# Kernel tuning notes

Measured on AMD Instinct MI355X. Metric: run time of the kernel, lower is better.

The kernel has to match this reference:

```python
import jax, jax.numpy as jnp
import numpy as np

EPS_BN = 1e-5
EPS_NORM = 1e-12


def _l2norm_c(x):
    # F.normalize over channel dim (dim=1) of [n, d, h, w]
    n = jnp.sqrt(jnp.sum(x * x, axis=1, keepdims=True))
    return x / jnp.maximum(n, EPS_NORM)


def setup_inputs() -> dict:
    key = jax.random.key(0)
    ks = jax.random.split(key, 8)
    g, p, d, h, w = 64, 64, 512, 24, 8
    hw = h * w
    return {
        "gal_fea": jax.random.normal(ks[0], (g, d, h, w), dtype=jnp.float32),
        "prob_fea": jax.random.normal(ks[1], (p, d, h, w), dtype=jnp.float32),
        "bn_weight": jax.random.uniform(ks[2], (1,), dtype=jnp.float32) + 0.5,
        "bn_bias": jax.random.uniform(ks[3], (1,), dtype=jnp.float32) - 0.5,
        "bn_mean": jnp.zeros((1,), dtype=jnp.float32),
        "bn_var": jnp.ones((1,), dtype=jnp.float32),
        "fc_weight": jax.random.normal(ks[4], (1, 2 * hw), dtype=jnp.float32) * 0.05,
        "fc_bias": jax.random.normal(ks[5], (1,), dtype=jnp.float32) * 0.05,
        "lbn_weight": jax.random.uniform(ks[6], (1,), dtype=jnp.float32) + 0.5,
        "lbn_bias": jax.random.uniform(ks[7], (1,), dtype=jnp.float32) - 0.5,
        "lbn_mean": jnp.zeros((1,), dtype=jnp.float32),
        "lbn_var": jnp.ones((1,), dtype=jnp.float32),
    }


def reference(gal_fea, prob_fea, bn_weight, bn_bias, bn_mean, bn_var,
              fc_weight, fc_bias, lbn_weight, lbn_bias, lbn_mean, lbn_var):
    g, d, h, w = gal_fea.shape
    p = prob_fea.shape[0]
    hw = h * w

    # L2-normalize over channels, flatten spatial dims
    gal = _l2norm_c(gal_fea).reshape(g, d, hw)              # [g, d, j]
    ker = _l2norm_c(prob_fea).transpose(0, 2, 3, 1).reshape(p, hw, d)  # [p, i, d]

    # cosine-similarity cross-correlation: s[g,p,i,j] = <probe pos i, gallery pos j>
    s = jnp.einsum('pid,gdj->gpij', ker, gal)               # [g, p, hw, hw]

    # dual spatial max-pool: max over probe positions, max over gallery positions
    score = jnp.concatenate([s.max(axis=2), s.max(axis=3)], axis=-1)  # [g, p, 2*hw]

    # eval-mode BatchNorm1d(1): scalar affine broadcast over all elements
    score = (score - bn_mean) / jnp.sqrt(bn_var + EPS_BN) * bn_weight + bn_bias

    # fc: Linear(2*hw, 1)
    score = jnp.einsum('gpk,ok->gpo', score, fc_weight)[..., 0] + fc_bias[0]  # [g, p]

    # eval-mode logit BatchNorm1d(1): scalar affine
    score = (score - lbn_mean) / jnp.sqrt(lbn_var + EPS_BN) * lbn_weight + lbn_bias

    return jax.nn.sigmoid(score / 10.0)
```

## Files before the change

kernel.cpp:

```cpp
#include <hip/hip_runtime.h>

#define HW 192
#define DD 512
#define GG 64
#define PP 64
#define SLAB 98304

typedef __attribute__((ext_vector_type(4))) int intx4;

__device__ __forceinline__ unsigned int pk4(float a, float b, float c, float d) {
  int qa = (int)rintf(a), qb = (int)rintf(b), qc = (int)rintf(c), qd = (int)rintf(d);
  return (unsigned)(qa & 255) | ((unsigned)(qb & 255) << 8) |
         ((unsigned)(qc & 255) << 16) | ((unsigned)(qd & 255) << 24);
}

__global__ __launch_bounds__(512, 2) void norm_kernel(
    const float* __restrict__ gal, const float* __restrict__ prob,
    unsigned char* __restrict__ ws) {
  int b = blockIdx.x;
  int s = b / 12;
  int q = b - s * 12;
  const float* in = (s < GG) ? (gal + (size_t)s * DD * HW)
                             : (prob + (size_t)(s - GG) * DD * HW);
  unsigned char* out = ws + (size_t)s * SLAB;
  int pos0 = q * 16;
  int t = threadIdx.x;

  __shared__ float T[16][524];
  __shared__ float sqa[128][17];
  __shared__ float sq2[16][17];
  __shared__ float scl[16];

  {
    int cq = t >> 2;
    int quad = t & 3;
    float p0 = 0.f, p1 = 0.f, p2 = 0.f, p3 = 0.f;
#pragma unroll
    for (int cb = 0; cb < 4; ++cb) {
      int c = cb * 128 + cq;
      const float4 v = *(const float4*)(in + (size_t)c * HW + pos0 + quad * 4);
      T[quad * 4 + 0][c] = v.x;
      T[quad * 4 + 1][c] = v.y;
      T[quad * 4 + 2][c] = v.z;
      T[quad * 4 + 3][c] = v.w;
      p0 += v.x * v.x; p1 += v.y * v.y; p2 += v.z * v.z; p3 += v.w * v.w;
    }
    sqa[cq][quad * 4 + 0] = p0;
    sqa[cq][quad * 4 + 1] = p1;
    sqa[cq][quad * 4 + 2] = p2;
    sqa[cq][quad * 4 + 3] = p3;
  }
  __syncthreads();
  if (t < 256) {
    int g2 = t >> 4, pos = t & 15;
    float v = 0.f;
#pragma unroll
    for (int r = 0; r < 8; ++r) v += sqa[g2 * 8 + r][pos];
    sq2[g2][pos] = v;
  }
  __syncthreads();
  if (t < 16) {
    float v = 0.f;
#pragma unroll
    for (int r = 0; r < 16; ++r) v += sq2[r][t];
    scl[t] = 1.f / fmaxf(sqrtf(v), 1e-12f);
  }
  __syncthreads();

  {
    int kb2 = t >> 6;
    int lane = t & 63;
    int l4 = lane >> 4;
    int pos = lane & 15;
    float sc = scl[pos] * 127.f;
    int base = kb2 * 64 + l4 * 16;
    const float4 r0 = *(const float4*)&T[pos][base + 0];
    const float4 r1 = *(const float4*)&T[pos][base + 4];
    const float4 r2 = *(const float4*)&T[pos][base + 8];
    const float4 r3 = *(const float4*)&T[pos][base + 12];
    uint4 u;
    u.x = pk4(r0.x * sc, r0.y * sc, r0.z * sc, r0.w * sc);
    u.y = pk4(r1.x * sc, r1.y * sc, r1.z * sc, r1.w * sc);
    u.z = pk4(r2.x * sc, r2.y * sc, r2.z * sc, r2.w * sc);
    u.w = pk4(r3.x * sc, r3.y * sc, r3.z * sc, r3.w * sc);
    *(uint4*)(out + (size_t)kb2 * 12288 + (size_t)q * 1024 + (size_t)lane * 16) = u;
  }
}

#define GLOAD_LDS16(gp, lp)                                              \
  __builtin_amdgcn_global_load_lds(                                      \
      (const __attribute__((address_space(1))) unsigned int*)(gp),       \
      (__attribute__((address_space(3))) unsigned int*)(lp), 16, 0, 0)

__global__ __launch_bounds__(256, 2) void qaconv_gemm(
    const unsigned char* __restrict__ ws, const float* __restrict__ fcw,
    const float* __restrict__ bnw, const float* __restrict__ bnb,
    const float* __restrict__ bnm, const float* __restrict__ bnv,
    const float* __restrict__ fcb, const float* __restrict__ lw,
    const float* __restrict__ lb, const float* __restrict__ lm,
    const float* __restrict__ lv, float* __restrict__ out) {
  int bid0 = blockIdx.x;
  int bid = ((bid0 & 7) << 9) + (bid0 >> 3);
  int sb = bid >> 6, li = bid & 63;
  int g = ((sb >> 3) << 3) + (li >> 3);
  int p = ((sb & 7) << 3) + (li & 7);
  const unsigned char* Bsrc = ws + (size_t)g * SLAB;
  const unsigned char* Asrc = ws + (size_t)(GG + p) * SLAB;

  __shared__ unsigned char sbuf[3][24576];

  int tid = threadIdx.x;
  int lane = tid & 63;
  int wave = tid >> 6;
  int wi = wave >> 1, wj = wave & 1;
  int l15 = lane & 15, l4 = lane >> 4;

  intx4 acc[6][6];
#pragma unroll
  for (int a = 0; a < 6; ++a)
#pragma unroll
    for (int c = 0; c < 6; ++c) acc[a][c] = (intx4){0, 0, 0, 0};

  const unsigned char* stgsrc =
      ((wave < 2) ? Asrc : Bsrc) + (size_t)((wave & 1) * 6) * 1024 +
      (size_t)lane * 16;
  int fbase = wave * 6;

#define STAGE(KB)                                                         \
  do {                                                                    \
    const unsigned char* s_ = stgsrc + (size_t)(KB)*12288;                \
    _Pragma("unroll") for (int i_ = 0; i_ < 6; ++i_) {                    \
      GLOAD_LDS16(s_ + i_ * 1024, &sbuf[(KB) % 3][(fbase + i_) * 1024]);  \
    }                                                                     \
  } while (0)

  intx4 aR[2][6], bR[2][6];

#define DSRD(KB, RB)                                                      \
  do {                                                                    \
    const unsigned char* cb_ = &sbuf[(KB) % 3][lane * 16];                \
    _Pragma("unroll") for (int i_ = 0; i_ < 6; ++i_) {                    \
      aR[RB][i_] = *(const intx4*)(cb_ + (wi * 6 + i_) * 1024);           \
      bR[RB][i_] = *(const intx4*)(cb_ + (12 + wj * 6 + i_) * 1024);      \
    }                                                                     \
  } while (0)

#define MFMAB(RB)                                                         \
  do {                                                                    \
    _Pragma("unroll") for (int jt_ = 0; jt_ < 6; ++jt_) {                 \
      intx4 bb = bR[RB][jt_];                                             \
      _Pragma("unroll") for (int it_ = 0; it_ < 6; ++it_)                 \
          acc[it_][jt_] = __builtin_amdgcn_mfma_i32_16x16x64_i8(          \
              aR[RB][it_], bb, acc[it_][jt_], 0, 0, 0);                   \
    }                                                                     \
  } while (0)

#define PHASE(KB, VMW)                                                    \
  do {                                                                    \
    asm volatile("s_waitcnt vmcnt(" #VMW ") lgkmcnt(0)" ::: "memory");    \
    __builtin_amdgcn_s_barrier();                                         \
    if ((KB) + 3 <= 7) STAGE((KB) + 3);                                   \
    if ((KB) + 1 <= 7) DSRD((KB) + 1, ((KB) + 1) & 1);                    \
    __builtin_amdgcn_s_setprio(1);                                        \
    MFMAB((KB)&1);                                                        \
    __builtin_amdgcn_s_setprio(0);                                        \
  } while (0)

  STAGE(0);
  STAGE(1);
  STAGE(2);
  asm volatile("s_waitcnt vmcnt(12)" ::: "memory");
  __builtin_amdgcn_s_barrier();
  DSRD(0, 0);

  PHASE(0, 6);
  PHASE(1, 6);
  PHASE(2, 6);
  PHASE(3, 6);
  PHASE(4, 6);
  PHASE(5, 6);
  PHASE(6, 0);
  PHASE(7, 0);

#undef STAGE
#undef DSRD
#undef MFMAB
#undef PHASE

  __syncthreads();

  float (*colpart)[HW] = (float (*)[HW]) & sbuf[0][0];
  float (*rowpart)[HW] = (float (*)[HW]) & sbuf[0][1536];
  float (*redbuf)[2] = (float (*)[2]) & sbuf[0][3072];

  const float inv = 1.f / 16129.f;
  int cm[6];
  int rm[6][4];
#pragma unroll
  for (int jt = 0; jt < 6; ++jt) cm[jt] = -2147483647;
#pragma unroll
  for (int it = 0; it < 6; ++it)
#pragma unroll
    for (int r = 0; r < 4; ++r) rm[it][r] = -2147483647;
#pragma unroll
  for (int it = 0; it < 6; ++it)
#pragma unroll
    for (int jt = 0; jt < 6; ++jt)
#pragma unroll
      for (int r = 0; r < 4; ++r) {
        int v = acc[it][jt][r];
        cm[jt] = max(cm[jt], v);
        rm[it][r] = max(rm[it][r], v);
      }

#pragma unroll
  for (int jt = 0; jt < 6; ++jt) {
    int v = cm[jt];
    v = max(v, __shfl_xor(v, 16, 64));
    v = max(v, __shfl_xor(v, 32, 64));
    if (lane < 16) colpart[wi][wj * 96 + jt * 16 + lane] = (float)v * inv;
  }
#pragma unroll
  for (int it = 0; it < 6; ++it)
#pragma unroll
    for (int r = 0; r < 4; ++r) {
      int v = rm[it][r];
      v = max(v, __shfl_xor(v, 1, 64));
      v = max(v, __shfl_xor(v, 2, 64));
      v = max(v, __shfl_xor(v, 4, 64));
      v = max(v, __shfl_xor(v, 8, 64));
      if (l15 == 0) rowpart[wj][wi * 96 + it * 16 + l4 * 4 + r] = (float)v * inv;
    }
  __syncthreads();

  float part = 0.f, wpart = 0.f;
  if (tid < HW) {
    float cmax = fmaxf(colpart[0][tid], colpart[1][tid]);
    float rmax = fmaxf(rowpart[0][tid], rowpart[1][tid]);
    float w1 = fcw[tid], w2 = fcw[HW + tid];
    part = cmax * w1 + rmax * w2;
    wpart = w1 + w2;
  }
#pragma unroll
  for (int off = 32; off > 0; off >>= 1) {
    part += __shfl_down(part, off, 64);
    wpart += __shfl_down(wpart, off, 64);
  }
  if (lane == 0) { redbuf[wave][0] = part; redbuf[wave][1] = wpart; }
  __syncthreads();
  if (tid == 0) {
    float s = redbuf[0][0] + redbuf[1][0] + redbuf[2][0] + redbuf[3][0];
    float wsum = redbuf[0][1] + redbuf[1][1] + redbuf[2][1] + redbuf[3][1];
    float bnA = bnw[0] * rsqrtf(bnv[0] + 1e-5f);
    float bnB = bnb[0] - bnm[0] * bnA;
    float sc = bnA * s + bnB * wsum + fcb[0];
    float lA = lw[0] * rsqrtf(lv[0] + 1e-5f);
    sc = (sc - lm[0]) * lA + lb[0];
    out[g * PP + p] = 1.f / (1.f + __expf(-sc * 0.1f));
  }
}

extern "C" void kernel_launch(void* const* d_in, const int* in_sizes, int n_in,
                              void* d_out, int out_size, void* d_ws, size_t ws_size,
                              hipStream_t stream) {
  const float* gal  = (const float*)d_in[0];
  const float* prob = (const float*)d_in[1];
  const float* bnw  = (const float*)d_in[2];
  const float* bnb  = (const float*)d_in[3];
  const float* bnm  = (const float*)d_in[4];
  const float* bnv  = (const float*)d_in[5];
  const float* fcw  = (const float*)d_in[6];
  const float* fcb  = (const float*)d_in[7];
  const float* lw   = (const float*)d_in[8];
  const float* lb   = (const float*)d_in[9];
  const float* lm   = (const float*)d_in[10];
  const float* lv   = (const float*)d_in[11];
  unsigned char* ws = (unsigned char*)d_ws;
  float* out = (float*)d_out;

  hipLaunchKernelGGL(norm_kernel, dim3(1536), dim3(512), 0, stream, gal, prob, ws);
  hipLaunchKernelGGL(qaconv_gemm, dim3(GG * PP), dim3(256), 0, stream, ws, fcw,
                     bnw, bnb, bnm, bnv, fcb, lw, lb, lm, lv, out);
}
```

Measured before the change: 212.0 us.

## Split GEMM work across eight waves with 6x3 tiles and shallower staging

```diff
diff --git a/kernel.cpp b/kernel.cpp
--- a/kernel.cpp
+++ b/kernel.cpp
@@ -92,7 +92,7 @@
       (const __attribute__((address_space(1))) unsigned int*)(gp),       \
       (__attribute__((address_space(3))) unsigned int*)(lp), 16, 0, 0)
 
-__global__ __launch_bounds__(256, 2) void qaconv_gemm(
+__global__ __launch_bounds__(512, 4) void qaconv_gemm(
     const unsigned char* __restrict__ ws, const float* __restrict__ fcw,
     const float* __restrict__ bnw, const float* __restrict__ bnb,
     const float* __restrict__ bnm, const float* __restrict__ bnv,
@@ -112,92 +112,90 @@
   int tid = threadIdx.x;
   int lane = tid & 63;
   int wave = tid >> 6;
-  int wi = wave >> 1, wj = wave & 1;
+  int wi = wave >> 2;
+  int wj = wave & 3;
   int l15 = lane & 15, l4 = lane >> 4;
 
-  intx4 acc[6][6];
+  intx4 acc[6][3];
 #pragma unroll
   for (int a = 0; a < 6; ++a)
 #pragma unroll
-    for (int c = 0; c < 6; ++c) acc[a][c] = (intx4){0, 0, 0, 0};
+    for (int c = 0; c < 3; ++c) acc[a][c] = (intx4){0, 0, 0, 0};
 
   const unsigned char* stgsrc =
-      ((wave < 2) ? Asrc : Bsrc) + (size_t)((wave & 1) * 6) * 1024 +
+      ((wave < 4) ? (Asrc + (size_t)(wave * 3) * 1024)
+                  : (Bsrc + (size_t)(wave * 3 - 12) * 1024)) +
       (size_t)lane * 16;
-  int fbase = wave * 6;
+  int fbase = wave * 3;
 
 #define STAGE(KB)                                                         \
   do {                                                                    \
     const unsigned char* s_ = stgsrc + (size_t)(KB)*12288;                \
-    _Pragma("unroll") for (int i_ = 0; i_ < 6; ++i_) {                    \
+    _Pragma("unroll") for (int i_ = 0; i_ < 3; ++i_) {                    \
       GLOAD_LDS16(s_ + i_ * 1024, &sbuf[(KB) % 3][(fbase + i_) * 1024]);  \
     }                                                                     \
   } while (0)
 
-  intx4 aR[2][6], bR[2][6];
-
-#define DSRD(KB, RB)                                                      \
+  intx4 a[6], b[3];
+
+#define DSRD(KB)                                                          \
   do {                                                                    \
     const unsigned char* cb_ = &sbuf[(KB) % 3][lane * 16];                \
-    _Pragma("unroll") for (int i_ = 0; i_ < 6; ++i_) {                    \
-      aR[RB][i_] = *(const intx4*)(cb_ + (wi * 6 + i_) * 1024);           \
-      bR[RB][i_] = *(const intx4*)(cb_ + (12 + wj * 6 + i_) * 1024);      \
-    }                                                                     \
-  } while (0)
-
-#define MFMAB(RB)                                                         \
-  do {                                                                    \
-    _Pragma("unroll") for (int jt_ = 0; jt_ < 6; ++jt_) {                 \
-      intx4 bb = bR[RB][jt_];                                             \
+    _Pragma("unroll") for (int i_ = 0; i_ < 6; ++i_)                      \
+        a[i_] = *(const intx4*)(cb_ + (wi * 6 + i_) * 1024);              \
+    _Pragma("unroll") for (int j_ = 0; j_ < 3; ++j_)                      \
+        b[j_] = *(const intx4*)(cb_ + (12 + wj * 3 + j_) * 1024);         \
+  } while (0)
+
+#define MFMA18()                                                          \
+  do {                                                                    \
+    _Pragma("unroll") for (int jt_ = 0; jt_ < 3; ++jt_) {                 \
+      intx4 bb = b[jt_];                                                  \
       _Pragma("unroll") for (int it_ = 0; it_ < 6; ++it_)                 \
           acc[it_][jt_] = __builtin_amdgcn_mfma_i32_16x16x64_i8(          \
-              aR[RB][it_], bb, acc[it_][jt_], 0, 0, 0);                   \
+              a[it_], bb, acc[it_][jt_], 0, 0, 0);                        \
     }                                                                     \
   } while (0)
 
 #define PHASE(KB, VMW)                                                    \
   do {                                                                    \
-    asm volatile("s_waitcnt vmcnt(" #VMW ") lgkmcnt(0)" ::: "memory");    \
+    asm volatile("s_waitcnt vmcnt(" #VMW ")" ::: "memory");               \
     __builtin_amdgcn_s_barrier();                                         \
-    if ((KB) + 3 <= 7) STAGE((KB) + 3);                                   \
-    if ((KB) + 1 <= 7) DSRD((KB) + 1, ((KB) + 1) & 1);                    \
+    if ((KB) + 2 <= 7) STAGE((KB) + 2);                                   \
+    DSRD(KB);                                                             \
     __builtin_amdgcn_s_setprio(1);                                        \
-    MFMAB((KB)&1);                                                        \
+    MFMA18();                                                             \
     __builtin_amdgcn_s_setprio(0);                                        \
   } while (0)
 
   STAGE(0);
   STAGE(1);
-  STAGE(2);
-  asm volatile("s_waitcnt vmcnt(12)" ::: "memory");
-  __builtin_amdgcn_s_barrier();
-  DSRD(0, 0);
-
-  PHASE(0, 6);
-  PHASE(1, 6);
-  PHASE(2, 6);
-  PHASE(3, 6);
-  PHASE(4, 6);
-  PHASE(5, 6);
-  PHASE(6, 0);
+
+  PHASE(0, 3);
+  PHASE(1, 3);
+  PHASE(2, 3);
+  PHASE(3, 3);
+  PHASE(4, 3);
+  PHASE(5, 3);
+  PHASE(6, 3);
   PHASE(7, 0);
 
 #undef STAGE
 #undef DSRD
-#undef MFMAB
+#undef MFMA18
 #undef PHASE
 
   __syncthreads();
 
   float (*colpart)[HW] = (float (*)[HW]) & sbuf[0][0];
   float (*rowpart)[HW] = (float (*)[HW]) & sbuf[0][1536];
-  float (*redbuf)[2] = (float (*)[2]) & sbuf[0][3072];
+  float (*redbuf)[2] = (float (*)[2]) & sbuf[0][4608];
 
   const float inv = 1.f / 16129.f;
-  int cm[6];
+  int cm[3];
   int rm[6][4];
 #pragma unroll
-  for (int jt = 0; jt < 6; ++jt) cm[jt] = -2147483647;
+  for (int jt = 0; jt < 3; ++jt) cm[jt] = -2147483647;
 #pragma unroll
   for (int it = 0; it < 6; ++it)
 #pragma unroll
@@ -205,7 +203,7 @@
 #pragma unroll
   for (int it = 0; it < 6; ++it)
 #pragma unroll
-    for (int jt = 0; jt < 6; ++jt)
+    for (int jt = 0; jt < 3; ++jt)
 #pragma unroll
       for (int r = 0; r < 4; ++r) {
         int v = acc[it][jt][r];
@@ -214,11 +212,11 @@
       }
 
 #pragma unroll
-  for (int jt = 0; jt < 6; ++jt) {
+  for (int jt = 0; jt < 3; ++jt) {
     int v = cm[jt];
     v = max(v, __shfl_xor(v, 16, 64));
     v = max(v, __shfl_xor(v, 32, 64));
-    if (lane < 16) colpart[wi][wj * 96 + jt * 16 + lane] = (float)v * inv;
+    if (lane < 16) colpart[wi][wj * 48 + jt * 16 + lane] = (float)v * inv;
   }
 #pragma unroll
   for (int it = 0; it < 6; ++it)
@@ -229,14 +227,16 @@
       v = max(v, __shfl_xor(v, 2, 64));
       v = max(v, __shfl_xor(v, 4, 64));
       v = max(v, __shfl_xor(v, 8, 64));
-      if (l15 == 0) rowpart[wj][wi * 96 + it * 16 + l4 * 4 + r] = (float)v * inv;
+      if (l15 == 0)
+        rowpart[wj][wi * 96 + it * 16 + l4 * 4 + r] = (float)v * inv;
     }
   __syncthreads();
 
   float part = 0.f, wpart = 0.f;
   if (tid < HW) {
     float cmax = fmaxf(colpart[0][tid], colpart[1][tid]);
-    float rmax = fmaxf(rowpart[0][tid], rowpart[1][tid]);
+    float rmax = fmaxf(fmaxf(rowpart[0][tid], rowpart[1][tid]),
+                       fmaxf(rowpart[2][tid], rowpart[3][tid]));
     float w1 = fcw[tid], w2 = fcw[HW + tid];
     part = cmax * w1 + rmax * w2;
     wpart = w1 + w2;
@@ -249,8 +249,9 @@
   if (lane == 0) { redbuf[wave][0] = part; redbuf[wave][1] = wpart; }
   __syncthreads();
   if (tid == 0) {
-    float s = redbuf[0][0] + redbuf[1][0] + redbuf[2][0] + redbuf[3][0];
-    float wsum = redbuf[0][1] + redbuf[1][1] + redbuf[2][1] + redbuf[3][1];
+    float s = 0.f, wsum = 0.f;
+#pragma unroll
+    for (int w = 0; w < 8; ++w) { s += redbuf[w][0]; wsum += redbuf[w][1]; }
     float bnA = bnw[0] * rsqrtf(bnv[0] + 1e-5f);
     float bnB = bnb[0] - bnm[0] * bnA;
     float sc = bnA * s + bnB * wsum + fcb[0];
@@ -279,6 +280,6 @@
   float* out = (float*)d_out;
 
   hipLaunchKernelGGL(norm_kernel, dim3(1536), dim3(512), 0, stream, gal, prob, ws);
-  hipLaunchKernelGGL(qaconv_gemm, dim3(GG * PP), dim3(256), 0, stream, ws, fcw,
+  hipLaunchKernelGGL(qaconv_gemm, dim3(GG * PP), dim3(512), 0, stream, ws, fcw,
                      bnw, bnb, bnm, bnv, fcb, lw, lb, lm, lv, out);
 }
```

After: 205.8 us. 1.03x faster.

## Interleave LDS reads with MFMA groups and shorten global prefetch depth

Applied to the files above, without the earlier changes.

```diff
diff --git a/kernel.cpp b/kernel.cpp
--- a/kernel.cpp
+++ b/kernel.cpp
@@ -136,56 +136,62 @@
 
   intx4 aR[2][6], bR[2][6];
 
-#define DSRD(KB, RB)                                                      \
+#define DSRD2(KB, RB, J)                                                  \
   do {                                                                    \
     const unsigned char* cb_ = &sbuf[(KB) % 3][lane * 16];                \
-    _Pragma("unroll") for (int i_ = 0; i_ < 6; ++i_) {                    \
-      aR[RB][i_] = *(const intx4*)(cb_ + (wi * 6 + i_) * 1024);           \
-      bR[RB][i_] = *(const intx4*)(cb_ + (12 + wj * 6 + i_) * 1024);      \
+    aR[RB][J] = *(const intx4*)(cb_ + (wi * 6 + (J)) * 1024);             \
+    bR[RB][J] = *(const intx4*)(cb_ + (12 + wj * 6 + (J)) * 1024);        \
+  } while (0)
+
+#define MFMAG(RB, JT)                                                     \
+  do {                                                                    \
+    intx4 bb = bR[RB][JT];                                                \
+    _Pragma("unroll") for (int it_ = 0; it_ < 6; ++it_)                   \
+        acc[it_][JT] = __builtin_amdgcn_mfma_i32_16x16x64_i8(             \
+            aR[RB][it_], bb, acc[it_][JT], 0, 0, 0);                      \
+  } while (0)
+
+#define SGB __builtin_amdgcn_sched_group_barrier
+
+#define PHASE(KB)                                                         \
+  do {                                                                    \
+    asm volatile("s_waitcnt vmcnt(0)" ::: "memory");                      \
+    __builtin_amdgcn_s_barrier();                                         \
+    if ((KB) + 2 <= 7) STAGE((KB) + 2);                                   \
+    __builtin_amdgcn_s_setprio(1);                                        \
+    _Pragma("unroll") for (int jt_ = 0; jt_ < 6; ++jt_) {                 \
+      if ((KB) + 1 <= 7) DSRD2((KB) + 1, ((KB) + 1) & 1, jt_);            \
+      MFMAG((KB)&1, jt_);                                                 \
     }                                                                     \
-  } while (0)
-
-#define MFMAB(RB)                                                         \
-  do {                                                                    \
+    __builtin_amdgcn_s_setprio(0);                                        \
+    if ((KB) + 2 <= 7) SGB(0x20, 6, 0);      \
     _Pragma("unroll") for (int jt_ = 0; jt_ < 6; ++jt_) {                 \
-      intx4 bb = bR[RB][jt_];                                             \
-      _Pragma("unroll") for (int it_ = 0; it_ < 6; ++it_)                 \
-          acc[it_][jt_] = __builtin_amdgcn_mfma_i32_16x16x64_i8(          \
-              aR[RB][it_], bb, acc[it_][jt_], 0, 0, 0);                   \
+      if ((KB) + 1 <= 7) SGB(0x100, 2, 0);                 \
+      SGB(0x8, 6, 0);                                         \
     }                                                                     \
-  } while (0)
-
-#define PHASE(KB, VMW)                                                    \
-  do {                                                                    \
-    asm volatile("s_waitcnt vmcnt(" #VMW ") lgkmcnt(0)" ::: "memory");    \
-    __builtin_amdgcn_s_barrier();                                         \
-    if ((KB) + 3 <= 7) STAGE((KB) + 3);                                   \
-    if ((KB) + 1 <= 7) DSRD((KB) + 1, ((KB) + 1) & 1);                    \
-    __builtin_amdgcn_s_setprio(1);                                        \
-    MFMAB((KB)&1);                                                        \
-    __builtin_amdgcn_s_setprio(0);                                        \
   } while (0)
 
   STAGE(0);
   STAGE(1);
-  STAGE(2);
-  asm volatile("s_waitcnt vmcnt(12)" ::: "memory");
+  asm volatile("s_waitcnt vmcnt(6)" ::: "memory");
   __builtin_amdgcn_s_barrier();
-  DSRD(0, 0);
-
-  PHASE(0, 6);
-  PHASE(1, 6);
-  PHASE(2, 6);
-  PHASE(3, 6);
-  PHASE(4, 6);
-  PHASE(5, 6);
-  PHASE(6, 0);
-  PHASE(7, 0);
+#pragma unroll
+  for (int j = 0; j < 6; ++j) DSRD2(0, 0, j);
+
+  PHASE(0);
+  PHASE(1);
+  PHASE(2);
+  PHASE(3);
+  PHASE(4);
+  PHASE(5);
+  PHASE(6);
+  PHASE(7);
 
 #undef STAGE
-#undef DSRD
-#undef MFMAB
+#undef DSRD2
+#undef MFMAG
 #undef PHASE
+#undef SGB
 
   __syncthreads();
 
```

Measured after the change: 196.6 us. 7.3% less time.
